# Performance work log

Hardware: AMD Instinct MI355X
Metric: run time of the kernel (lower is better)

Reference implementation:

```python
import jax, jax.numpy as jnp
import numpy as np

EMB = 768
HEADS = 12
HEAD_DIM = EMB // HEADS
SEQ = 4096
BATCH = 1


def setup_inputs() -> dict:
    key = jax.random.key(0)
    ks = jax.random.split(key, 9)
    s = 1.0 / np.sqrt(EMB)
    return {
        "x": jax.random.normal(ks[0], (BATCH, SEQ, EMB), dtype=jnp.float32),
        "wq": jax.random.normal(ks[1], (EMB, EMB), dtype=jnp.float32) * s,
        "bq": jax.random.normal(ks[2], (EMB,), dtype=jnp.float32) * s,
        "wk": jax.random.normal(ks[3], (EMB, EMB), dtype=jnp.float32) * s,
        "bk": jax.random.normal(ks[4], (EMB,), dtype=jnp.float32) * s,
        "wv": jax.random.normal(ks[5], (EMB, EMB), dtype=jnp.float32) * s,
        "bv": jax.random.normal(ks[6], (EMB,), dtype=jnp.float32) * s,
        "wo": jax.random.normal(ks[7], (EMB, EMB), dtype=jnp.float32) * s,
        "bo": jax.random.normal(ks[8], (EMB,), dtype=jnp.float32) * s,
    }


def reference(x, wq, bq, wk, bk, wv, bv, wo, bo):
    b, n, _ = x.shape
    # projections: [b, n, emb] -> [b, heads, n, head_dim]
    def split_heads(t):
        return t.reshape(b, n, HEADS, HEAD_DIM).transpose(0, 2, 1, 3)
    q = split_heads(x @ wq + bq)
    k = split_heads(x @ wk + bk)
    v = split_heads(x @ wv + bv)
    # full N x N scores (naive attention, as in the original)
    scores = jnp.einsum("bhqd,bhkd->bhqk", q, k)
    causal = jnp.triu(jnp.ones((n, n), dtype=bool), k=1)
    scores = jnp.where(causal, -jnp.inf, scores)
    weights = jax.nn.softmax(scores / np.sqrt(HEAD_DIM), axis=-1)
    # dropout with rate 0.0 is identity (eval mode)
    ctx = jnp.einsum("bhqk,bhkd->bhqd", weights, v)
    ctx = ctx.transpose(0, 2, 1, 3).reshape(b, n, EMB)
    return ctx @ wo + bo
```

## Files before the change

### kernel.cpp

```cpp
#include <hip/hip_runtime.h>
#include <stdint.h>

#define SEQ 4096
#define EMB 768
#define HEADS 12
#define HD 64

typedef __attribute__((ext_vector_type(8))) short short8;
typedef __attribute__((ext_vector_type(4))) short short4v;
typedef __attribute__((ext_vector_type(8))) __bf16 bf16x8;
typedef __attribute__((ext_vector_type(4))) __bf16 bf16x4;
typedef __attribute__((ext_vector_type(4))) float f32x4;

#define QSCALE 0.18033688011112043f

static __device__ __forceinline__ unsigned short f2bf(float f) {
    unsigned int u = __builtin_bit_cast(unsigned int, f);
    unsigned int r = 0x7fffu + ((u >> 16) & 1u);
    u += r;
    return (unsigned short)(u >> 16);
}

static __device__ __forceinline__ f32x4 mfma32(short8 a, short8 b, f32x4 c) {
    return __builtin_amdgcn_mfma_f32_16x16x32_bf16(
        __builtin_bit_cast(bf16x8, a), __builtin_bit_cast(bf16x8, b), c, 0, 0, 0);
}

static __device__ __forceinline__ f32x4 mfma16(short4v a, short4v b, f32x4 c) {
#if __has_builtin(__builtin_amdgcn_mfma_f32_16x16x16_bf16)
    return __builtin_amdgcn_mfma_f32_16x16x16_bf16(
        __builtin_bit_cast(bf16x4, a), __builtin_bit_cast(bf16x4, b), c, 0, 0, 0);
#else
    return __builtin_amdgcn_mfma_f32_16x16x16bf16_1k(a, b, c, 0, 0, 0);
#endif
}

static __device__ __forceinline__ short4v pack4bf(float a, float b, float c, float d) {
#if __has_builtin(__builtin_amdgcn_cvt_pk_bf16_f32)
    typedef __attribute__((ext_vector_type(2))) __bf16 bf16x2;
    bf16x2 lo = __builtin_amdgcn_cvt_pk_bf16_f32(a, b);
    bf16x2 hi = __builtin_amdgcn_cvt_pk_bf16_f32(c, d);
    uint2 u = {__builtin_bit_cast(unsigned int, lo), __builtin_bit_cast(unsigned int, hi)};
    return __builtin_bit_cast(short4v, u);
#else
    short4v p;
    p[0] = (short)f2bf(a); p[1] = (short)f2bf(b);
    p[2] = (short)f2bf(c); p[3] = (short)f2bf(d);
    return p;
#endif
}

static __device__ __forceinline__ void load_lds16(const void* g, void* l) {
    __builtin_amdgcn_global_load_lds(
        (const __attribute__((address_space(1))) unsigned int*)(uintptr_t)g,
        (__attribute__((address_space(3))) unsigned int*)(uintptr_t)l, 16, 0, 0);
}

static __device__ __forceinline__ int pid_of(int h, int i128, int ch) {
    int b = (i128 < 20) ? (i128 - 10)
                        : (i128 < 30 ? 10 + (i128 - 20) * 2 : 30 + (i128 - 30) * 3);
    return h * 36 + b + (ch - 1);
}

static __device__ __forceinline__ void softmax_step(f32x4* st, float& m_i, float& l_i,
                                                    f32x4* O, short4v* pk) {
    float mx = -3.0e38f;
    for (int nt = 0; nt < 4; nt++)
        for (int r = 0; r < 4; r++) mx = fmaxf(mx, st[nt][r]);
    mx = fmaxf(mx, __shfl_xor(mx, 16));
    mx = fmaxf(mx, __shfl_xor(mx, 32));
    const bool inc = mx > m_i;
    if (__ballot(inc)) {
        const float mn = inc ? mx : m_i;
        const float alpha = __builtin_amdgcn_exp2f(m_i - mn);
        m_i = mn;
        l_i *= alpha;
        for (int dt = 0; dt < 4; dt++)
            for (int r = 0; r < 4; r++) O[dt][r] *= alpha;
    }
    float rs = 0.f;
    for (int nt = 0; nt < 4; nt++) {
        float p0 = __builtin_amdgcn_exp2f(st[nt][0] - m_i);
        float p1 = __builtin_amdgcn_exp2f(st[nt][1] - m_i);
        float p2 = __builtin_amdgcn_exp2f(st[nt][2] - m_i);
        float p3 = __builtin_amdgcn_exp2f(st[nt][3] - m_i);
        rs += p0 + p1 + p2 + p3;
        pk[nt] = pack4bf(p0, p1, p2, p3);
    }
    rs += __shfl_xor(rs, 16);
    rs += __shfl_xor(rs, 32);
    l_i += rs;
}

__global__ __launch_bounds__(256) void convert_all(const float* __restrict__ x,
                                                   const float* __restrict__ wq,
                                                   const float* __restrict__ wk,
                                                   const float* __restrict__ wv,
                                                   const float* __restrict__ wo,
                                                   unsigned short* __restrict__ xb,
                                                   unsigned short* __restrict__ wqkvT,
                                                   unsigned short* __restrict__ woT) {
    __shared__ float Ls[64][65];
    const int bid = blockIdx.x;
    if (bid < 3072) {
        int i = bid * 256 + threadIdx.x;
        float4 v = ((const float4*)x)[i];
        ushort4 o = {f2bf(v.x), f2bf(v.y), f2bf(v.z), f2bf(v.w)};
        ((ushort4*)xb)[i] = o;
        return;
    }
    const int idx = bid - 3072;
    const int z = idx / 144;
    const int bx = (idx % 144) / 12, by = idx % 12;
    const float* W = (z == 0) ? wq : (z == 1) ? wk : (z == 2) ? wv : wo;
    unsigned short* dst = (z < 3) ? (wqkvT + (size_t)z * EMB * EMB) : woT;
    const int k0 = bx * 64, n0 = by * 64;
    const int r = threadIdx.x >> 2, c0 = (threadIdx.x & 3) * 16;
    for (int j = 0; j < 16; j += 4) {
        float4 v = *(const float4*)&W[(size_t)(k0 + r) * EMB + n0 + c0 + j];
        Ls[r][c0 + j] = v.x;
        Ls[r][c0 + j + 1] = v.y;
        Ls[r][c0 + j + 2] = v.z;
        Ls[r][c0 + j + 3] = v.w;
    }
    __syncthreads();
    unsigned short tmp[16];
    for (int j = 0; j < 16; j++) tmp[j] = f2bf(Ls[c0 + j][r]);
    *(uint4*)&dst[(size_t)(n0 + r) * EMB + k0 + c0] = *(uint4*)tmp;
    *(uint4*)&dst[(size_t)(n0 + r) * EMB + k0 + c0 + 8] = *(uint4*)(tmp + 8);
}

__global__ __launch_bounds__(256) void gemm_qkv(const unsigned short* __restrict__ A,
                                                const unsigned short* __restrict__ Bt,
                                                const float* __restrict__ b0p,
                                                const float* __restrict__ b1p,
                                                const float* __restrict__ b2p,
                                                unsigned short* __restrict__ QKb,
                                                unsigned short* __restrict__ Vtb) {
    __shared__ __align__(16) unsigned short SMEM[16384];
    unsigned short* As0 = SMEM;
    unsigned short* Bs0 = SMEM + 4096;
    unsigned short* As1 = SMEM + 8192;
    unsigned short* Bs1 = SMEM + 12288;
    const int tid = threadIdx.x;
    const int wave = tid >> 6, lane = tid & 63, quad = lane >> 4, l16 = lane & 15;
    const int m0 = blockIdx.x * 128, n0 = blockIdx.y * 128;
    const int wm = (wave >> 1) * 64, wn = (wave & 1) * 64;
    const int lrow = lane >> 2, lcol = (lane & 3) * 8;

    f32x4 acc[4][4] = {};

    for (int k0 = 0; k0 < EMB; k0 += 64) {
        __syncthreads();
        for (int t = 0; t < 2; t++) {
            int row = wave * 32 + t * 16 + lrow;
            load_lds16(&A[(size_t)(m0 + row) * EMB + k0 + lcol], &As0[(wave * 2 + t) * 512]);
            load_lds16(&Bt[(size_t)(n0 + row) * EMB + k0 + lcol], &Bs0[(wave * 2 + t) * 512]);
            load_lds16(&A[(size_t)(m0 + row) * EMB + k0 + 32 + lcol], &As1[(wave * 2 + t) * 512]);
            load_lds16(&Bt[(size_t)(n0 + row) * EMB + k0 + 32 + lcol], &Bs1[(wave * 2 + t) * 512]);
        }
        __syncthreads();
        {
            short8 a[4], b[4];
            for (int i = 0; i < 4; i++)
                a[i] = *(const short8*)&As0[(wm + i * 16 + l16) * 32 + quad * 8];
            for (int i = 0; i < 4; i++)
                b[i] = *(const short8*)&Bs0[(wn + i * 16 + l16) * 32 + quad * 8];
            for (int i = 0; i < 4; i++)
                for (int j = 0; j < 4; j++) acc[i][j] = mfma32(a[i], b[j], acc[i][j]);
        }
        {
            short8 a[4], b[4];
            for (int i = 0; i < 4; i++)
                a[i] = *(const short8*)&As1[(wm + i * 16 + l16) * 32 + quad * 8];
            for (int i = 0; i < 4; i++)
                b[i] = *(const short8*)&Bs1[(wn + i * 16 + l16) * 32 + quad * 8];
            for (int i = 0; i < 4; i++)
                for (int j = 0; j < 4; j++) acc[i][j] = mfma32(a[i], b[j], acc[i][j]);
        }
    }

    const int z = n0 / EMB;
    if (z < 2) {
        const float* bias = z ? b1p : b0p;
        const float sc = z ? 1.0f : QSCALE;
        for (int i = 0; i < 4; i++)
            for (int j = 0; j < 4; j++) {
                int mbase = m0 + wm + i * 16 + quad * 4;
                int n = n0 + wn + j * 16 + l16;
                float bv = bias[n - z * EMB];
                for (int r = 0; r < 4; r++)
                    QKb[(size_t)(mbase + r) * 1536 + n] = f2bf((acc[i][j][r] + bv) * sc);
            }
    } else {
        const int nn = n0 + wn + l16 - 2 * EMB;
        for (int j = 0; j < 4; j++) {
            __syncthreads();
            const float bv = b2p[nn + j * 16];
            const int nloc = (wave & 1) * 16 + l16;
            for (int i = 0; i < 4; i++) {
                ushort4 pk;
                pk.x = f2bf(acc[i][j][0] + bv);
                pk.y = f2bf(acc[i][j][1] + bv);
                pk.z = f2bf(acc[i][j][2] + bv);
                pk.w = f2bf(acc[i][j][3] + bv);
                *(ushort4*)&SMEM[nloc * 136 + wm + i * 16 + quad * 4] = pk;
            }
            __syncthreads();
            const int nl = tid >> 3, c = tid & 7;
            const int ng = (nl >> 4) * 64 + j * 16 + (nl & 15) + n0 - 2 * EMB;
            const int hh = ng >> 6, dd = ng & 63;
            unsigned short* dst = &Vtb[(size_t)(hh * HD + dd) * SEQ + m0];
            *(uint4*)&dst[c * 8] = *(uint4*)&SMEM[nl * 136 + c * 8];
            *(uint4*)&dst[64 + c * 8] = *(uint4*)&SMEM[nl * 136 + 64 + c * 8];
        }
    }
}

__global__ __launch_bounds__(256) void gemm_out(const unsigned short* __restrict__ A,
                                                const unsigned short* __restrict__ Bt,
                                                const float* __restrict__ bias,
                                                float* __restrict__ outp) {
    __shared__ __align__(16) unsigned short SMEM[12288];
    unsigned short* As0 = SMEM;
    unsigned short* As1 = SMEM + 2048;
    unsigned short* Bs0 = SMEM + 4096;
    unsigned short* Bs1 = SMEM + 8192;
    const int tid = threadIdx.x;
    const int wave = tid >> 6, lane = tid & 63, quad = lane >> 4, l16 = lane & 15;
    const int m0 = blockIdx.x * 64, n0 = blockIdx.y * 128;
    const int wm = (wave >> 1) * 32, wn = (wave & 1) * 64;
    const int lrow = lane >> 2, lcol = (lane & 3) * 8;

    f32x4 acc[2][4] = {};

    for (int k0 = 0; k0 < EMB; k0 += 64) {
        __syncthreads();
        load_lds16(&A[(size_t)(m0 + wave * 16 + lrow) * EMB + k0 + lcol], &As0[wave * 512]);
        load_lds16(&A[(size_t)(m0 + wave * 16 + lrow) * EMB + k0 + 32 + lcol], &As1[wave * 512]);
        for (int t = 0; t < 2; t++) {
            int row = wave * 32 + t * 16 + lrow;
            load_lds16(&Bt[(size_t)(n0 + row) * EMB + k0 + lcol], &Bs0[(wave * 2 + t) * 512]);
            load_lds16(&Bt[(size_t)(n0 + row) * EMB + k0 + 32 + lcol], &Bs1[(wave * 2 + t) * 512]);
        }
        __syncthreads();
        {
            short8 a[2], b[4];
            for (int i = 0; i < 2; i++)
                a[i] = *(const short8*)&As0[(wm + i * 16 + l16) * 32 + quad * 8];
            for (int j = 0; j < 4; j++)
                b[j] = *(const short8*)&Bs0[(wn + j * 16 + l16) * 32 + quad * 8];
            for (int i = 0; i < 2; i++)
                for (int j = 0; j < 4; j++) acc[i][j] = mfma32(a[i], b[j], acc[i][j]);
        }
        {
            short8 a[2], b[4];
            for (int i = 0; i < 2; i++)
                a[i] = *(const short8*)&As1[(wm + i * 16 + l16) * 32 + quad * 8];
            for (int j = 0; j < 4; j++)
                b[j] = *(const short8*)&Bs1[(wn + j * 16 + l16) * 32 + quad * 8];
            for (int i = 0; i < 2; i++)
                for (int j = 0; j < 4; j++) acc[i][j] = mfma32(a[i], b[j], acc[i][j]);
        }
    }

    for (int i = 0; i < 2; i++)
        for (int j = 0; j < 4; j++) {
            int mbase = m0 + wm + i * 16 + quad * 4;
            int n = n0 + wn + j * 16 + l16;
            float bv = bias[n];
            for (int r = 0; r < 4; r++) outp[(size_t)(mbase + r) * EMB + n] = acc[i][j][r] + bv;
        }
}

__global__ __launch_bounds__(512) void attn_kernel(const unsigned short* __restrict__ QKb,
                                                   const unsigned short* __restrict__ Vtb,
                                                   unsigned short* __restrict__ ctxb,
                                                   unsigned short* __restrict__ Op,
                                                   float* __restrict__ mArr,
                                                   float* __restrict__ lArr) {
    __shared__ __align__(16) unsigned short Ks[64 * 64];
    __shared__ __align__(16) unsigned short Vs[64 * 64];

    const int bid = blockIdx.x;
    const int h = bid % HEADS;
    const int r2 = 67 - bid / HEADS;
    int i128, ch, nch;
    if (r2 < 10) {
        i128 = r2; ch = 0; nch = 1;
    } else if (r2 < 30) {
        int t = r2 - 10; i128 = 10 + (t >> 1); ch = t & 1; nch = 2;
    } else if (r2 < 60) {
        int t = r2 - 30; i128 = 20 + t / 3; ch = t % 3; nch = 3;
    } else {
        int t = r2 - 60; i128 = 30 + (t >> 2); ch = t & 3; nch = 4;
    }
    const int T = 2 * i128 + 2;
    const int kb = ch * T / nch;
    const int ke = (ch + 1) * T / nch - 1;
    const int qbase = i128 * 128;
    const int tid = threadIdx.x;
    const int wave = tid >> 6, lane = tid & 63, quad = lane >> 4, l16 = lane & 15;

    const unsigned short* Qg = QKb + (size_t)h * HD;
    const unsigned short* Kg = QKb + (size_t)(EMB + h * HD);
    const unsigned short* Vh = Vtb + (size_t)h * HD * SEQ;

    const int q = qbase + wave * 16 + l16;
    const short8 bQ0 = *(const short8*)&Qg[(size_t)q * 1536 + quad * 8];
    const short8 bQ1 = *(const short8*)&Qg[(size_t)q * 1536 + 32 + quad * 8];

    const int row = tid >> 3, t8 = tid & 7;
    const int swk = row & 7, swv = row & 15;

    f32x4 O[4] = {};
    float m_i = -3.0e38f, l_i = 0.f;

    uint4 kr, vr;
    {
        const int kb64 = kb * 64;
        kr = *(const uint4*)&Kg[(size_t)(kb64 + row) * 1536 + t8 * 8];
        vr = *(const uint4*)&Vh[(size_t)row * SEQ + kb64 + t8 * 8];
    }

    for (int kt = kb; kt <= ke; kt++) {
        const int kbase = kt * 64;
        __syncthreads();
        *(uint4*)&Ks[row * 64 + (t8 ^ swk) * 8] = kr;
        *(uint2*)&Vs[row * 64 + ((2 * t8) ^ swv) * 4] = ((const uint2*)&vr)[0];
        *(uint2*)&Vs[row * 64 + ((2 * t8 + 1) ^ swv) * 4] = ((const uint2*)&vr)[1];
        if (kt < ke) {
            const int nb = kbase + 64;
            kr = *(const uint4*)&Kg[(size_t)(nb + row) * 1536 + t8 * 8];
            vr = *(const uint4*)&Vh[(size_t)row * SEQ + nb + t8 * 8];
        }
        __syncthreads();

        if (kbase > qbase + wave * 16 + 15) continue;

        const int swr = l16 & 7;
        f32x4 st[4];
        for (int nt = 0; nt < 4; nt++) {
            short8 aK0 = *(const short8*)&Ks[(nt * 16 + l16) * 64 + (quad ^ swr) * 8];
            short8 aK1 = *(const short8*)&Ks[(nt * 16 + l16) * 64 + ((quad + 4) ^ swr) * 8];
            f32x4 z = {};
            z = mfma32(aK0, bQ0, z);
            z = mfma32(aK1, bQ1, z);
            st[nt] = z;
        }
        if (kbase + 63 > qbase + wave * 16) {
            for (int nt = 0; nt < 4; nt++)
                for (int r = 0; r < 4; r++)
                    if (kbase + nt * 16 + quad * 4 + r > q) st[nt][r] = -INFINITY;
        }

        short4v pk[4];
        softmax_step(st, m_i, l_i, O, pk);

        for (int dt = 0; dt < 4; dt++)
            for (int nt = 0; nt < 4; nt++) {
                short4v av =
                    *(const short4v*)&Vs[(dt * 16 + l16) * 64 + ((4 * nt + quad) ^ l16) * 4];
                O[dt] = mfma16(av, pk[nt], O[dt]);
            }
    }

    const int ql = wave * 16 + l16;
    if (nch == 1) {
        const float inv = 1.f / l_i;
        for (int dt = 0; dt < 4; dt++) {
            ushort4 o;
            o.x = f2bf(O[dt][0] * inv);
            o.y = f2bf(O[dt][1] * inv);
            o.z = f2bf(O[dt][2] * inv);
            o.w = f2bf(O[dt][3] * inv);
            *(ushort4*)&ctxb[(size_t)q * EMB + h * HD + dt * 16 + quad * 4] = o;
        }
    } else {
        if (ch == 0) {
            for (int dt = 0; dt < 4; dt++) {
                ushort4 o;
                o.x = f2bf(O[dt][0]);
                o.y = f2bf(O[dt][1]);
                o.z = f2bf(O[dt][2]);
                o.w = f2bf(O[dt][3]);
                *(ushort4*)&ctxb[(size_t)q * EMB + h * HD + dt * 16 + quad * 4] = o;
            }
        } else {
            const int pid = pid_of(h, i128, ch);
            for (int dt = 0; dt < 4; dt++) {
                ushort4 o;
                o.x = f2bf(O[dt][0]);
                o.y = f2bf(O[dt][1]);
                o.z = f2bf(O[dt][2]);
                o.w = f2bf(O[dt][3]);
                *(ushort4*)&Op[(size_t)pid * 8192 + ql * 64 + dt * 16 + quad * 4] = o;
            }
        }
        if (quad == 0) {
            const int mli = ((h * 32 + i128) * 4 + ch) * 128 + ql;
            mArr[mli] = m_i;
            lArr[mli] = l_i;
        }
    }
}

__global__ __launch_bounds__(256) void merge_kernel(const unsigned short* __restrict__ Op,
                                                    const float* __restrict__ mArr,
                                                    const float* __restrict__ lArr,
                                                    unsigned short* __restrict__ ctxb) {
    const int gid = blockIdx.x;
    const int h = gid % HEADS;
    const int i128 = 10 + gid / HEADS;
    const int nch = (i128 < 20) ? 2 : (i128 < 30) ? 3 : 4;
    const int q = threadIdx.x >> 1, d0 = (threadIdx.x & 1) * 32;
    const int mlbase = (h * 32 + i128) * 4;

    float mc[4], lc[4];
    for (int c = 0; c < nch; c++) {
        mc[c] = mArr[(mlbase + c) * 128 + q];
        lc[c] = lArr[(mlbase + c) * 128 + q];
    }
    float M = mc[0];
    for (int c = 1; c < nch; c++) M = fmaxf(M, mc[c]);
    float w[4], L = 0.f;
    for (int c = 0; c < nch; c++) {
        w[c] = __builtin_amdgcn_exp2f(mc[c] - M);
        L += w[c] * lc[c];
    }
    const float inv = 1.f / L;
    for (int c = 0; c < nch; c++) w[c] *= inv;

    unsigned short* dst = &ctxb[(size_t)(i128 * 128 + q) * EMB + h * HD + d0];
    for (int jj = 0; jj < 32; jj += 8) {
        uint4 u0 = *(const uint4*)&dst[jj];
        float f[8];
        const unsigned short* p0 = (const unsigned short*)&u0;
        for (int t = 0; t < 8; t++)
            f[t] = w[0] * __builtin_bit_cast(float, (unsigned int)p0[t] << 16);
        for (int c = 1; c < nch; c++) {
            const int pid = pid_of(h, i128, c);
            uint4 u = *(const uint4*)&Op[(size_t)pid * 8192 + q * 64 + d0 + jj];
            const unsigned short* p = (const unsigned short*)&u;
            for (int t = 0; t < 8; t++)
                f[t] += w[c] * __builtin_bit_cast(float, (unsigned int)p[t] << 16);
        }
        unsigned short o[8];
        for (int t = 0; t < 8; t++) o[t] = f2bf(f[t]);
        *(uint4*)&dst[jj] = *(uint4*)o;
    }
}

extern "C" void kernel_launch(void* const* d_in, const int* in_sizes, int n_in,
                              void* d_out, int out_size, void* d_ws, size_t ws_size,
                              hipStream_t stream) {
    const float* x = (const float*)d_in[0];
    const float* wq = (const float*)d_in[1];
    const float* bq = (const float*)d_in[2];
    const float* wk = (const float*)d_in[3];
    const float* bk = (const float*)d_in[4];
    const float* wv = (const float*)d_in[5];
    const float* bv = (const float*)d_in[6];
    const float* wo = (const float*)d_in[7];
    const float* bo = (const float*)d_in[8];

    unsigned short* ws = (unsigned short*)d_ws;
    unsigned short* xb = ws;
    unsigned short* wqkvT = xb + SEQ * EMB;
    unsigned short* woT = wqkvT + 3 * EMB * EMB;
    unsigned short* QKb = woT + EMB * EMB;
    unsigned short* Vtb = QKb + (size_t)SEQ * 1536;
    unsigned short* ctxb = Vtb + HEADS * SEQ * HD;
    unsigned short* Op = xb;
    float* mArr = (float*)(ws + 3538944);
    float* lArr = mArr + 196608;

    convert_all<<<dim3(3072 + 576), 256, 0, stream>>>(x, wq, wk, wv, wo, xb, wqkvT, woT);
    gemm_qkv<<<dim3(SEQ / 128, 3 * EMB / 128), 256, 0, stream>>>(
        xb, wqkvT, bq, bk, bv, QKb, Vtb);
    attn_kernel<<<dim3(12 * 68), 512, 0, stream>>>(QKb, Vtb, ctxb, Op, mArr, lArr);
    merge_kernel<<<dim3(264), 256, 0, stream>>>(Op, mArr, lArr, ctxb);
    gemm_out<<<dim3(SEQ / 64, EMB / 128), 256, 0, stream>>>(ctxb, woT, bo, (float*)d_out);
}
```

Before: 193.2 us.

## Double-buffer LDS tiles with direct global-to-LDS prefetch in GEMMs and attention

Both GEMM kernels switch to ping-pong LDS buffers with a K step of 32: the next tile is prefetched into the other buffer while MFMAs consume the current one, so each iteration needs one barrier instead of two. The attention kernel drops register staging of K/V and uses load_lds16 into double-buffered Ks/Vs. It also changes the V swizzle to an 8-row XOR pattern, with the read indexing adjusted to match. This aims to overlap memory latency with compute and cut barriers, at the cost of twice the LDS in attention and more GEMM loop iterations. It relies on async LDS loads being complete at the next barrier.

```diff
diff --git a/kernel.cpp b/kernel.cpp
--- a/kernel.cpp
+++ b/kernel.cpp
@@ -138,10 +138,6 @@
                                                 unsigned short* __restrict__ QKb,
                                                 unsigned short* __restrict__ Vtb) {
     __shared__ __align__(16) unsigned short SMEM[16384];
-    unsigned short* As0 = SMEM;
-    unsigned short* Bs0 = SMEM + 4096;
-    unsigned short* As1 = SMEM + 8192;
-    unsigned short* Bs1 = SMEM + 12288;
     const int tid = threadIdx.x;
     const int wave = tid >> 6, lane = tid & 63, quad = lane >> 4, l16 = lane & 15;
     const int m0 = blockIdx.x * 128, n0 = blockIdx.y * 128;
@@ -150,34 +146,31 @@
 
     f32x4 acc[4][4] = {};
 
-    for (int k0 = 0; k0 < EMB; k0 += 64) {
+    for (int t = 0; t < 2; t++) {
+        int row = wave * 32 + t * 16 + lrow;
+        load_lds16(&A[(size_t)(m0 + row) * EMB + lcol], &SMEM[(wave * 2 + t) * 512]);
+        load_lds16(&Bt[(size_t)(n0 + row) * EMB + lcol], &SMEM[4096 + (wave * 2 + t) * 512]);
+    }
+    int buf = 0;
+    for (int k0 = 0; k0 < EMB; k0 += 32) {
         __syncthreads();
-        for (int t = 0; t < 2; t++) {
-            int row = wave * 32 + t * 16 + lrow;
-            load_lds16(&A[(size_t)(m0 + row) * EMB + k0 + lcol], &As0[(wave * 2 + t) * 512]);
-            load_lds16(&Bt[(size_t)(n0 + row) * EMB + k0 + lcol], &Bs0[(wave * 2 + t) * 512]);
-            load_lds16(&A[(size_t)(m0 + row) * EMB + k0 + 32 + lcol], &As1[(wave * 2 + t) * 512]);
-            load_lds16(&Bt[(size_t)(n0 + row) * EMB + k0 + 32 + lcol], &Bs1[(wave * 2 + t) * 512]);
-        }
-        __syncthreads();
-        {
-            short8 a[4], b[4];
-            for (int i = 0; i < 4; i++)
-                a[i] = *(const short8*)&As0[(wm + i * 16 + l16) * 32 + quad * 8];
-            for (int i = 0; i < 4; i++)
-                b[i] = *(const short8*)&Bs0[(wn + i * 16 + l16) * 32 + quad * 8];
-            for (int i = 0; i < 4; i++)
-                for (int j = 0; j < 4; j++) acc[i][j] = mfma32(a[i], b[j], acc[i][j]);
-        }
-        {
-            short8 a[4], b[4];
-            for (int i = 0; i < 4; i++)
-                a[i] = *(const short8*)&As1[(wm + i * 16 + l16) * 32 + quad * 8];
-            for (int i = 0; i < 4; i++)
-                b[i] = *(const short8*)&Bs1[(wn + i * 16 + l16) * 32 + quad * 8];
-            for (int i = 0; i < 4; i++)
-                for (int j = 0; j < 4; j++) acc[i][j] = mfma32(a[i], b[j], acc[i][j]);
-        }
+        if (k0 + 32 < EMB) {
+            unsigned short* A_ = &SMEM[(buf ^ 1) * 8192];
+            unsigned short* B_ = A_ + 4096;
+            for (int t = 0; t < 2; t++) {
+                int row = wave * 32 + t * 16 + lrow;
+                load_lds16(&A[(size_t)(m0 + row) * EMB + k0 + 32 + lcol], &A_[(wave * 2 + t) * 512]);
+                load_lds16(&Bt[(size_t)(n0 + row) * EMB + k0 + 32 + lcol], &B_[(wave * 2 + t) * 512]);
+            }
+        }
+        const unsigned short* A_ = &SMEM[buf * 8192];
+        const unsigned short* B_ = A_ + 4096;
+        short8 a[4], b[4];
+        for (int i = 0; i < 4; i++) a[i] = *(const short8*)&A_[(wm + i * 16 + l16) * 32 + quad * 8];
+        for (int i = 0; i < 4; i++) b[i] = *(const short8*)&B_[(wn + i * 16 + l16) * 32 + quad * 8];
+        for (int i = 0; i < 4; i++)
+            for (int j = 0; j < 4; j++) acc[i][j] = mfma32(a[i], b[j], acc[i][j]);
+        buf ^= 1;
     }
 
     const int z = n0 / EMB;
@@ -222,10 +215,6 @@
                                                 const float* __restrict__ bias,
                                                 float* __restrict__ outp) {
     __shared__ __align__(16) unsigned short SMEM[12288];
-    unsigned short* As0 = SMEM;
-    unsigned short* As1 = SMEM + 2048;
-    unsigned short* Bs0 = SMEM + 4096;
-    unsigned short* Bs1 = SMEM + 8192;
     const int tid = threadIdx.x;
     const int wave = tid >> 6, lane = tid & 63, quad = lane >> 4, l16 = lane & 15;
     const int m0 = blockIdx.x * 64, n0 = blockIdx.y * 128;
@@ -234,34 +223,31 @@
 
     f32x4 acc[2][4] = {};
 
-    for (int k0 = 0; k0 < EMB; k0 += 64) {
+    load_lds16(&A[(size_t)(m0 + wave * 16 + lrow) * EMB + lcol], &SMEM[wave * 512]);
+    for (int t = 0; t < 2; t++) {
+        int row = wave * 32 + t * 16 + lrow;
+        load_lds16(&Bt[(size_t)(n0 + row) * EMB + lcol], &SMEM[4096 + (wave * 2 + t) * 512]);
+    }
+    int buf = 0;
+    for (int k0 = 0; k0 < EMB; k0 += 32) {
         __syncthreads();
-        load_lds16(&A[(size_t)(m0 + wave * 16 + lrow) * EMB + k0 + lcol], &As0[wave * 512]);
-        load_lds16(&A[(size_t)(m0 + wave * 16 + lrow) * EMB + k0 + 32 + lcol], &As1[wave * 512]);
-        for (int t = 0; t < 2; t++) {
-            int row = wave * 32 + t * 16 + lrow;
-            load_lds16(&Bt[(size_t)(n0 + row) * EMB + k0 + lcol], &Bs0[(wave * 2 + t) * 512]);
-            load_lds16(&Bt[(size_t)(n0 + row) * EMB + k0 + 32 + lcol], &Bs1[(wave * 2 + t) * 512]);
-        }
-        __syncthreads();
-        {
-            short8 a[2], b[4];
-            for (int i = 0; i < 2; i++)
-                a[i] = *(const short8*)&As0[(wm + i * 16 + l16) * 32 + quad * 8];
-            for (int j = 0; j < 4; j++)
-                b[j] = *(const short8*)&Bs0[(wn + j * 16 + l16) * 32 + quad * 8];
-            for (int i = 0; i < 2; i++)
-                for (int j = 0; j < 4; j++) acc[i][j] = mfma32(a[i], b[j], acc[i][j]);
-        }
-        {
-            short8 a[2], b[4];
-            for (int i = 0; i < 2; i++)
-                a[i] = *(const short8*)&As1[(wm + i * 16 + l16) * 32 + quad * 8];
-            for (int j = 0; j < 4; j++)
-                b[j] = *(const short8*)&Bs1[(wn + j * 16 + l16) * 32 + quad * 8];
-            for (int i = 0; i < 2; i++)
-                for (int j = 0; j < 4; j++) acc[i][j] = mfma32(a[i], b[j], acc[i][j]);
-        }
+        if (k0 + 32 < EMB) {
+            unsigned short* A_ = &SMEM[(buf ^ 1) * 2048];
+            unsigned short* B_ = &SMEM[4096 + (buf ^ 1) * 4096];
+            load_lds16(&A[(size_t)(m0 + wave * 16 + lrow) * EMB + k0 + 32 + lcol], &A_[wave * 512]);
+            for (int t = 0; t < 2; t++) {
+                int row = wave * 32 + t * 16 + lrow;
+                load_lds16(&Bt[(size_t)(n0 + row) * EMB + k0 + 32 + lcol], &B_[(wave * 2 + t) * 512]);
+            }
+        }
+        const unsigned short* A_ = &SMEM[buf * 2048];
+        const unsigned short* B_ = &SMEM[4096 + buf * 4096];
+        short8 a[2], b[4];
+        for (int i = 0; i < 2; i++) a[i] = *(const short8*)&A_[(wm + i * 16 + l16) * 32 + quad * 8];
+        for (int j = 0; j < 4; j++) b[j] = *(const short8*)&B_[(wn + j * 16 + l16) * 32 + quad * 8];
+        for (int i = 0; i < 2; i++)
+            for (int j = 0; j < 4; j++) acc[i][j] = mfma32(a[i], b[j], acc[i][j]);
+        buf ^= 1;
     }
 
     for (int i = 0; i < 2; i++)
@@ -279,8 +265,8 @@
                                                    unsigned short* __restrict__ Op,
                                                    float* __restrict__ mArr,
                                                    float* __restrict__ lArr) {
-    __shared__ __align__(16) unsigned short Ks[64 * 64];
-    __shared__ __align__(16) unsigned short Vs[64 * 64];
+    __shared__ __align__(16) unsigned short Ks[2][64 * 64];
+    __shared__ __align__(16) unsigned short Vs[2][64 * 64];
 
     const int bid = blockIdx.x;
     const int h = bid % HEADS;
@@ -310,59 +296,56 @@
     const short8 bQ0 = *(const short8*)&Qg[(size_t)q * 1536 + quad * 8];
     const short8 bQ1 = *(const short8*)&Qg[(size_t)q * 1536 + 32 + quad * 8];
 
-    const int row = tid >> 3, t8 = tid & 7;
-    const int swk = row & 7, swv = row & 15;
+    const int srow = wave * 8 + ((lane >> 3));
+    const int sg = (lane & 7) ^ (srow & 7);
 
     f32x4 O[4] = {};
     float m_i = -3.0e38f, l_i = 0.f;
 
-    uint4 kr, vr;
     {
         const int kb64 = kb * 64;
-        kr = *(const uint4*)&Kg[(size_t)(kb64 + row) * 1536 + t8 * 8];
-        vr = *(const uint4*)&Vh[(size_t)row * SEQ + kb64 + t8 * 8];
-    }
-
+        load_lds16(&Kg[(size_t)(kb64 + srow) * 1536 + sg * 8], &Ks[0][wave * 512]);
+        load_lds16(&Vh[(size_t)srow * SEQ + kb64 + sg * 8], &Vs[0][wave * 512]);
+    }
+    int buf = 0;
     for (int kt = kb; kt <= ke; kt++) {
         const int kbase = kt * 64;
         __syncthreads();
-        *(uint4*)&Ks[row * 64 + (t8 ^ swk) * 8] = kr;
-        *(uint2*)&Vs[row * 64 + ((2 * t8) ^ swv) * 4] = ((const uint2*)&vr)[0];
-        *(uint2*)&Vs[row * 64 + ((2 * t8 + 1) ^ swv) * 4] = ((const uint2*)&vr)[1];
         if (kt < ke) {
             const int nb = kbase + 64;
-            kr = *(const uint4*)&Kg[(size_t)(nb + row) * 1536 + t8 * 8];
-            vr = *(const uint4*)&Vh[(size_t)row * SEQ + nb + t8 * 8];
-        }
-        __syncthreads();
-
-        if (kbase > qbase + wave * 16 + 15) continue;
-
-        const int swr = l16 & 7;
-        f32x4 st[4];
-        for (int nt = 0; nt < 4; nt++) {
-            short8 aK0 = *(const short8*)&Ks[(nt * 16 + l16) * 64 + (quad ^ swr) * 8];
-            short8 aK1 = *(const short8*)&Ks[(nt * 16 + l16) * 64 + ((quad + 4) ^ swr) * 8];
-            f32x4 z = {};
-            z = mfma32(aK0, bQ0, z);
-            z = mfma32(aK1, bQ1, z);
-            st[nt] = z;
-        }
-        if (kbase + 63 > qbase + wave * 16) {
-            for (int nt = 0; nt < 4; nt++)
-                for (int r = 0; r < 4; r++)
-                    if (kbase + nt * 16 + quad * 4 + r > q) st[nt][r] = -INFINITY;
-        }
-
-        short4v pk[4];
-        softmax_step(st, m_i, l_i, O, pk);
-
-        for (int dt = 0; dt < 4; dt++)
+            load_lds16(&Kg[(size_t)(nb + srow) * 1536 + sg * 8], &Ks[buf ^ 1][wave * 512]);
+            load_lds16(&Vh[(size_t)srow * SEQ + nb + sg * 8], &Vs[buf ^ 1][wave * 512]);
+        }
+        if (kbase <= qbase + wave * 16 + 15) {
+            const int swr = l16 & 7;
+            f32x4 st[4];
             for (int nt = 0; nt < 4; nt++) {
-                short4v av =
-                    *(const short4v*)&Vs[(dt * 16 + l16) * 64 + ((4 * nt + quad) ^ l16) * 4];
-                O[dt] = mfma16(av, pk[nt], O[dt]);
-            }
+                short8 aK0 = *(const short8*)&Ks[buf][(nt * 16 + l16) * 64 + (quad ^ swr) * 8];
+                short8 aK1 =
+                    *(const short8*)&Ks[buf][(nt * 16 + l16) * 64 + ((quad + 4) ^ swr) * 8];
+                f32x4 z = {};
+                z = mfma32(aK0, bQ0, z);
+                z = mfma32(aK1, bQ1, z);
+                st[nt] = z;
+            }
+            if (kbase + 63 > qbase + wave * 16) {
+                for (int nt = 0; nt < 4; nt++)
+                    for (int r = 0; r < 4; r++)
+                        if (kbase + nt * 16 + quad * 4 + r > q) st[nt][r] = -INFINITY;
+            }
+
+            short4v pk[4];
+            softmax_step(st, m_i, l_i, O, pk);
+
+            for (int dt = 0; dt < 4; dt++)
+                for (int nt = 0; nt < 4; nt++) {
+                    const int j = 4 * nt + quad;
+                    short4v av = *(const short4v*)&Vs[buf][(dt * 16 + l16) * 64 +
+                                                          (2 * ((j >> 1) ^ swr) + (j & 1)) * 4];
+                    O[dt] = mfma16(av, pk[nt], O[dt]);
+                }
+        }
+        buf ^= 1;
     }
 
     const int ql = wave * 16 + l16;
```

Result: no change. 194.8 us (+0.8%).
